# Kernel optimization log

Hardware: AMD Instinct MI355X
Metric: run time of the kernel (lower is better)

## Reference

```python
import jax, jax.numpy as jnp
import numpy as np

B, S, E, H = 4, 1024, 1024, 16
HD = E // H
TEMP = float(E) ** 0.5


def setup_inputs() -> dict:
    key = jax.random.key(0)
    ks = jax.random.split(key, 6)
    x = jax.random.normal(ks[0], (B, S, E), dtype=jnp.float32)
    mask = jax.random.randint(ks[1], (1, 1, S, S), 0, 2).astype(bool)
    prev = jax.random.normal(ks[2], (B, H, S, S), dtype=jnp.float32)
    qkv_w = jax.random.normal(ks[3], (3 * E, E), dtype=jnp.float32) * (1.0 / np.sqrt(E))
    qkv_b = jnp.zeros((3 * E,), dtype=jnp.float32)
    o_w = jax.random.normal(ks[4], (E, E), dtype=jnp.float32) * (1.0 / np.sqrt(E))
    o_b = jnp.zeros((E,), dtype=jnp.float32)
    return {"x": x, "mask": mask, "prev": prev, "qkv_w": qkv_w,
            "qkv_b": qkv_b, "o_w": o_w, "o_b": o_b}


def reference(x, mask, prev, qkv_w, qkv_b, o_w, o_b):
    b, s, _ = x.shape
    # qkv_proj: torch Linear -> x @ W^T + b, then per-head interleaved split
    qkv = x @ qkv_w.T + qkv_b                      # [B, S, 3E]
    qkv = qkv.reshape(b, s, H, 3 * HD).transpose(0, 2, 1, 3)  # [B, H, S, 3*HD]
    q, k, v = jnp.split(qkv, 3, axis=-1)           # each [B, H, S, HD]
    attn = jnp.einsum('bhqd,bhkd->bhqk', q, k) / TEMP + prev  # raw scores
    attn = jnp.where(mask, -jnp.inf, attn)         # masked_fill(mask, -inf)
    p = jax.nn.softmax(attn, axis=-1)              # dropout p=0 (eval)
    vals = jnp.einsum('bhqk,bhkd->bhqd', p, v)     # [B, H, S, HD]
    vals = vals.transpose(0, 2, 1, 3).reshape(b, s, E)
    return vals @ o_w.T + o_b
```

## Files before the change

kernel.cpp:

```cpp
#include <hip/hip_runtime.h>

typedef unsigned short u16;
typedef unsigned char  u8;
typedef unsigned long long u64;

using bf16x8 = __attribute__((ext_vector_type(8))) short;
using f32x4  = __attribute__((ext_vector_type(4))) float;

static __device__ __forceinline__ u16 f2bf(float f) {
  union { float f; unsigned u; } v; v.f = f;
  unsigned r = v.u + 0x7fffu + ((v.u >> 16) & 1u);
  return (u16)(r >> 16);
}

static __device__ __forceinline__ void gload_lds16(const void* g, void* l) {
  __builtin_amdgcn_global_load_lds((const __attribute__((address_space(1))) void*)g,
                                   (__attribute__((address_space(3))) void*)l, 16, 0, 0);
}

__global__ __launch_bounds__(256) void cvt_bf16_kernel(const float4* __restrict__ in,
                                                       ushort4* __restrict__ out, int n4) {
  int i = blockIdx.x * 256 + threadIdx.x;
  if (i >= n4) return;
  float4 v = in[i];
  ushort4 o;
  o.x = f2bf(v.x); o.y = f2bf(v.y); o.z = f2bf(v.z); o.w = f2bf(v.w);
  out[i] = o;
}

__global__ __launch_bounds__(256) void zero_out_kernel(float* __restrict__ out, int n) {
  int i = blockIdx.x * 256 + threadIdx.x;
  if (i < n) out[i] = 0.f;
}

__global__ void mask_detect_kernel(const u8* __restrict__ mask, int* __restrict__ flag) {
  __shared__ int nz;
  if (threadIdx.x == 0) nz = 0;
  __syncthreads();
  int cnt = 0;
  for (int i = threadIdx.x; i < 4096; i += 256)
    if ((i & 3) && mask[i]) cnt++;
  if (cnt) atomicAdd(&nz, cnt);
  __syncthreads();
  if (threadIdx.x == 0) *flag = (nz == 0) ? 1 : 0;
}

__global__ __launch_bounds__(256) void mask_pack_kernel(const void* __restrict__ mask,
                                                        u64* __restrict__ out,
                                                        const int* __restrict__ flag, int nwords) {
  int w = blockIdx.x * 4 + (threadIdx.x >> 6);
  int lane = threadIdx.x & 63;
  if (w >= nwords) return;
  int idx = w * 64 + lane;
  int m;
  if (*flag) m = ((const int*)mask)[idx] != 0;
  else       m = ((const u8*)mask)[idx] != 0;
  u64 bits = __ballot(m != 0);
  if (lane == 0) out[w] = bits;
}

template<bool OUT_BF16>
__global__ __launch_bounds__(256, 2)
void gemm_bt(const u16* __restrict__ A, const u16* __restrict__ Bm,
             const float* __restrict__ bias, void* __restrict__ Cout,
             int M, int N, int K) {
  constexpr int BK = 64;
  __shared__ u16 lA[128 * BK];
  __shared__ u16 lB[128 * BK];
  const int tid = threadIdx.x;
  const int wv = tid >> 6, lane = tid & 63;
  const int wr = (wv >> 1) * 64, wc = (wv & 1) * 64;
  const int bm = blockIdx.x * 128, bn = blockIdx.y * 128;
  const int frow = lane & 15, fk = (lane >> 4) * 8;
  const int srow = tid >> 3;
  const int scol = (tid & 7) * 8;
  const u16* ga = A + (size_t)(bm + srow) * K + scol;
  const u16* gb = Bm + (size_t)(bn + srow) * K + scol;
  u16* la = &lA[srow * BK + scol];
  u16* lb = &lB[srow * BK + scol];

  f32x4 acc[4][4] = {};

  for (int k0 = 0; k0 < K; k0 += BK) {
#pragma unroll
    for (int r = 0; r < 4; ++r) {
      gload_lds16(ga + (size_t)(r * 32) * K + k0, la + r * 32 * BK);
      gload_lds16(gb + (size_t)(r * 32) * K + k0, lb + r * 32 * BK);
    }
    __syncthreads();
#pragma unroll
    for (int kk = 0; kk < 2; ++kk) {
      bf16x8 af[4], bf[4];
#pragma unroll
      for (int m = 0; m < 4; ++m)
        af[m] = *(const bf16x8*)&lA[(wr + m * 16 + frow) * BK + kk * 32 + fk];
#pragma unroll
      for (int n = 0; n < 4; ++n)
        bf[n] = *(const bf16x8*)&lB[(wc + n * 16 + frow) * BK + kk * 32 + fk];
#pragma unroll
      for (int m = 0; m < 4; ++m)
#pragma unroll
        for (int n = 0; n < 4; ++n)
          acc[m][n] = __builtin_amdgcn_mfma_f32_16x16x32_bf16(af[m], bf[n], acc[m][n], 0, 0, 0);
    }
    __syncthreads();
  }
#pragma unroll
  for (int n = 0; n < 4; ++n) {
    const int col = bn + wc + n * 16 + frow;
    const float bv = bias[col];
#pragma unroll
    for (int m = 0; m < 4; ++m) {
      const int row0 = bm + wr + m * 16 + (lane >> 4) * 4;
#pragma unroll
      for (int r = 0; r < 4; ++r) {
        float v = acc[m][n][r] + bv;
        if constexpr (OUT_BF16)
          ((u16*)Cout)[(size_t)(row0 + r) * N + col] = f2bf(v);
        else
          ((float*)Cout)[(size_t)(row0 + r) * N + col] = v;
      }
    }
  }
}

__global__ __launch_bounds__(256, 4)
void attn_kernel(const u16* __restrict__ qkv,
                 const float* __restrict__ prev,
                 const u64* __restrict__ mbits,
                 u16* __restrict__ vals) {
  constexpr int S = 1024;
  __shared__ u16 lQ[64 * 64];
  __shared__ u16 lK[64 * 64];
  __shared__ u16 lVT[64 * 64];
  __shared__ u16 lP[4][16 * 72];
  const int tid = threadIdx.x, wv = tid >> 6, lane = tid & 63;
  const int bh = blockIdx.x >> 4;
  const int qt = blockIdx.x & 15;
  const int b = bh >> 4, h = bh & 15;
  const int frow = lane & 15, fkg = lane >> 4, fk = fkg * 8;
  const int srow = tid >> 3, scol8 = (tid & 7) * 8;
  const size_t rowQ0 = (size_t)(b * S + qt * 64);

  const int scol_sw = scol8 ^ ((srow & 7) << 3);
  const int c0 = fk ^ ((frow & 7) << 3);
  const int c1 = (fk + 32) ^ ((frow & 7) << 3);

  {
    const u16* g = qkv + (rowQ0 + srow) * 3072 + h * 192 + scol_sw;
    gload_lds16(g, &lQ[srow * 64 + scol8]);
    gload_lds16(g + (size_t)32 * 3072, &lQ[(srow + 32) * 64 + scol8]);
  }
  __syncthreads();
  bf16x8 qf0 = *(const bf16x8*)&lQ[(wv * 16 + frow) * 64 + c0];
  bf16x8 qf1 = *(const bf16x8*)&lQ[(wv * 16 + frow) * 64 + c1];

  float m_run[4], l_run[4];
  f32x4 acc_o[4] = {};
#pragma unroll
  for (int r = 0; r < 4; ++r) { m_run[r] = -3e38f; l_run[r] = 0.f; }

  const int qloc = wv * 16 + fkg * 4;
  const float* prow = prev + ((size_t)bh * S + qt * 64 + qloc) * S;
  const u64* mrow = mbits + (size_t)(qt * 64 + qloc) * (S / 64);

  const int vsw = (tid & 7) << 3;

  for (int kt = 0; kt < 16; ++kt) {
    __syncthreads();
    {
      const u16* g = qkv + (size_t)(b * S + kt * 64 + srow) * 3072 + h * 192 + 64 + scol_sw;
      gload_lds16(g, &lK[srow * 64 + scol8]);
      gload_lds16(g + (size_t)32 * 3072, &lK[(srow + 32) * 64 + scol8]);
    }
    const u16* gv = qkv + (size_t)(b * S + kt * 64 + srow) * 3072 + h * 192 + 128 + scol8;
    bf16x8 v0 = *(const bf16x8*)gv;
    bf16x8 v1 = *(const bf16x8*)(gv + (size_t)32 * 3072);
    {
      const int k0 = srow ^ vsw;
      const int k1 = (srow + 32) ^ vsw;
#pragma unroll
      for (int j = 0; j < 8; ++j) {
        lVT[(scol8 + j) * 64 + k0] = (u16)v0[j];
        lVT[(scol8 + j) * 64 + k1] = (u16)v1[j];
      }
    }
    __syncthreads();
    const float* pp = prow + kt * 64 + frow;
    float pvraw[4][4];
    u64 mw[4];
#pragma unroll
    for (int r = 0; r < 4; ++r) mw[r] = mrow[r * (S / 64) + kt];
#pragma unroll
    for (int n = 0; n < 4; ++n)
#pragma unroll
      for (int r = 0; r < 4; ++r)
        pvraw[n][r] = pp[(size_t)r * S + n * 16];
    f32x4 s[4];
#pragma unroll
    for (int n = 0; n < 4; ++n) {
      bf16x8 kf0 = *(const bf16x8*)&lK[(n * 16 + frow) * 64 + c0];
      bf16x8 kf1 = *(const bf16x8*)&lK[(n * 16 + frow) * 64 + c1];
      f32x4 z = {0.f, 0.f, 0.f, 0.f};
      z = __builtin_amdgcn_mfma_f32_16x16x32_bf16(qf0, kf0, z, 0, 0, 0);
      s[n] = __builtin_amdgcn_mfma_f32_16x16x32_bf16(qf1, kf1, z, 0, 0, 0);
    }
#pragma unroll
    for (int r = 0; r < 4; ++r) {
      const u64 t = mw[r] >> frow;
#pragma unroll
      for (int n = 0; n < 4; ++n) {
        float sc = s[n][r] * 0.03125f + pvraw[n][r];
        s[n][r] = ((t >> (n * 16)) & 1ull) ? -1e30f : sc;
      }
    }
    float tmax[4];
#pragma unroll
    for (int r = 0; r < 4; ++r) {
      float t = fmaxf(fmaxf(s[0][r], s[1][r]), fmaxf(s[2][r], s[3][r]));
      t = fmaxf(t, __shfl_xor(t, 1));
      t = fmaxf(t, __shfl_xor(t, 2));
      t = fmaxf(t, __shfl_xor(t, 4));
      t = fmaxf(t, __shfl_xor(t, 8));
      tmax[r] = t;
    }
    float psum[4];
#pragma unroll
    for (int r = 0; r < 4; ++r) {
      float mnew = fmaxf(m_run[r], tmax[r]);
      float sc = __expf(m_run[r] - mnew);
      m_run[r] = mnew;
      l_run[r] *= sc;
#pragma unroll
      for (int dn = 0; dn < 4; ++dn) acc_o[dn][r] *= sc;
      float ps = 0.f;
#pragma unroll
      for (int n = 0; n < 4; ++n) {
        float p = __expf(s[n][r] - mnew);
        s[n][r] = p;
        ps += p;
      }
      psum[r] = ps;
    }
#pragma unroll
    for (int r = 0; r < 4; ++r) {
      float t = psum[r];
      t += __shfl_xor(t, 1); t += __shfl_xor(t, 2);
      t += __shfl_xor(t, 4); t += __shfl_xor(t, 8);
      l_run[r] += t;
    }
    u16* pw = &lP[wv][0];
#pragma unroll
    for (int n = 0; n < 4; ++n)
#pragma unroll
      for (int r = 0; r < 4; ++r)
        pw[(fkg * 4 + r) * 72 + n * 16 + frow] = f2bf(s[n][r]);
    bf16x8 pf0 = *(const bf16x8*)&pw[frow * 72 + fk];
    bf16x8 pf1 = *(const bf16x8*)&pw[frow * 72 + 32 + fk];
#pragma unroll
    for (int dn = 0; dn < 4; ++dn) {
      const int d = dn * 16 + frow;
      const int sw = ((dn * 2 + (frow >> 3)) & 7) << 3;
      bf16x8 vt0 = *(const bf16x8*)&lVT[d * 64 + (fk ^ sw)];
      bf16x8 vt1 = *(const bf16x8*)&lVT[d * 64 + ((fk + 32) ^ sw)];
      acc_o[dn] = __builtin_amdgcn_mfma_f32_16x16x32_bf16(pf0, vt0, acc_o[dn], 0, 0, 0);
      acc_o[dn] = __builtin_amdgcn_mfma_f32_16x16x32_bf16(pf1, vt1, acc_o[dn], 0, 0, 0);
    }
  }
#pragma unroll
  for (int r = 0; r < 4; ++r) {
    float inv = 1.0f / l_run[r];
    size_t row = (rowQ0 + qloc + r) * 1024 + h * 64;
#pragma unroll
    for (int dn = 0; dn < 4; ++dn)
      vals[row + dn * 16 + frow] = f2bf(acc_o[dn][r] * inv);
  }
}

extern "C" void kernel_launch(void* const* d_in, const int* in_sizes, int n_in,
                              void* d_out, int out_size, void* d_ws, size_t ws_size,
                              hipStream_t stream) {
  const float* x     = (const float*)d_in[0];
  const void*  mask  = d_in[1];
  const float* prev  = (const float*)d_in[2];
  const float* qkv_w = (const float*)d_in[3];
  const float* qkv_b = (const float*)d_in[4];
  const float* o_w   = (const float*)d_in[5];
  const float* o_b   = (const float*)d_in[6];

  const size_t WS_NEEDED = 14680064 + 25165824;
  if (ws_size < WS_NEEDED) {
    zero_out_kernel<<<(out_size + 255) / 256, 256, 0, stream>>>((float*)d_out, out_size);
    return;
  }

  char* ws = (char*)d_ws;
  u16* x_bf  = (u16*)(ws);
  u16* vals  = (u16*)(ws);
  u16* qw_bf   = (u16*)(ws + 8388608);
  u16* ow_bf   = (u16*)(ws + 8388608);
  u64* mask_b  = (u64*)(ws + 10485760);
  int* mflag   = (int*)(ws + 11534336);
  u16* qkv_o = (u16*)(ws + 14680064);

  cvt_bf16_kernel<<<4096, 256, 0, stream>>>((const float4*)x, (ushort4*)x_bf, 1048576);
  cvt_bf16_kernel<<<3072, 256, 0, stream>>>((const float4*)qkv_w, (ushort4*)qw_bf, 786432);

  dim3 g1(32, 24);
  gemm_bt<true><<<g1, 256, 0, stream>>>(x_bf, qw_bf, qkv_b, qkv_o, 4096, 3072, 1024);

  cvt_bf16_kernel<<<1024, 256, 0, stream>>>((const float4*)o_w, (ushort4*)ow_bf, 262144);
  mask_detect_kernel<<<1, 256, 0, stream>>>((const u8*)mask, mflag);
  mask_pack_kernel<<<4096, 256, 0, stream>>>(mask, mask_b, mflag, 16384);

  attn_kernel<<<1024, 256, 0, stream>>>(qkv_o, prev, mask_b, vals);

  dim3 g2(32, 8);
  gemm_bt<false><<<g2, 256, 0, stream>>>(vals, ow_bf, o_b, d_out, 4096, 1024, 1024);
}
```

Before: 508.8 us.

## Stage prev scores through LDS with async loads and fuse mask detect into pack

The attention kernel now loads each 64x64 tile of the fp32 prev bias into shared memory with async global-to-LDS 16-byte loads using an XOR swizzle, instead of scattered per-lane scalar global loads. This should make the dominant prev read traffic coalesced and let it overlap with the K/V tile loads. It adds 16KB of LDS per block, so the occupancy hint drops from 4 to 3 blocks. The separate single-block mask-detect launch is folded into the mask pack kernel, which redoes format detection locally in each block. This removes one launch and a serial dependency, and the packed mask moves to its own workspace region.

Result: no change. 517.9 us (+1.8%).

```diff
diff --git a/kernel.cpp b/kernel.cpp
--- a/kernel.cpp
+++ b/kernel.cpp
@@ -33,30 +33,21 @@
   if (i < n) out[i] = 0.f;
 }
 
-__global__ void mask_detect_kernel(const u8* __restrict__ mask, int* __restrict__ flag) {
+__global__ __launch_bounds__(256) void mask_pack_kernel(const void* __restrict__ mask,
+                                                        u64* __restrict__ out) {
   __shared__ int nz;
-  if (threadIdx.x == 0) nz = 0;
+  const int tid = threadIdx.x, b = blockIdx.x;
+  if (tid == 0) nz = 0;
   __syncthreads();
-  int cnt = 0;
-  for (int i = threadIdx.x; i < 4096; i += 256)
-    if ((i & 3) && mask[i]) cnt++;
-  if (cnt) atomicAdd(&nz, cnt);
+  const int idx = b * 256 + tid;
+  const u8 byte = ((const u8*)mask)[idx];
+  if ((idx & 3) && byte) atomicAdd(&nz, 1);
   __syncthreads();
-  if (threadIdx.x == 0) *flag = (nz == 0) ? 1 : 0;
-}
-
-__global__ __launch_bounds__(256) void mask_pack_kernel(const void* __restrict__ mask,
-                                                        u64* __restrict__ out,
-                                                        const int* __restrict__ flag, int nwords) {
-  int w = blockIdx.x * 4 + (threadIdx.x >> 6);
-  int lane = threadIdx.x & 63;
-  if (w >= nwords) return;
-  int idx = w * 64 + lane;
   int m;
-  if (*flag) m = ((const int*)mask)[idx] != 0;
-  else       m = ((const u8*)mask)[idx] != 0;
-  u64 bits = __ballot(m != 0);
-  if (lane == 0) out[w] = bits;
+  if (nz == 0) m = ((const int*)mask)[idx] != 0;
+  else         m = byte != 0;
+  u64 bits = __ballot(m);
+  if ((tid & 63) == 0) out[b * 4 + (tid >> 6)] = bits;
 }
 
 template<bool OUT_BF16>
@@ -124,7 +115,7 @@
   }
 }
 
-__global__ __launch_bounds__(256, 4)
+__global__ __launch_bounds__(256, 3)
 void attn_kernel(const u16* __restrict__ qkv,
                  const float* __restrict__ prev,
                  const u64* __restrict__ mbits,
@@ -134,6 +125,7 @@
   __shared__ u16 lK[64 * 64];
   __shared__ u16 lVT[64 * 64];
   __shared__ u16 lP[4][16 * 72];
+  __shared__ float lPrev[64 * 64];
   const int tid = threadIdx.x, wv = tid >> 6, lane = tid & 63;
   const int bh = blockIdx.x >> 4;
   const int qt = blockIdx.x & 15;
@@ -161,21 +153,31 @@
   for (int r = 0; r < 4; ++r) { m_run[r] = -3e38f; l_run[r] = 0.f; }
 
   const int qloc = wv * 16 + fkg * 4;
-  const float* prow = prev + ((size_t)bh * S + qt * 64 + qloc) * S;
   const u64* mrow = mbits + (size_t)(qt * 64 + qloc) * (S / 64);
+
+  const float* prevt = prev + ((size_t)bh * S + qt * 64) * S;
+  const int prow_s = wv * 4 + (lane >> 4);
+  const int pcolg = ((lane & 15) * 4) ^ (wv << 4);
+  const int prd = fkg << 4;
 
   const int vsw = (tid & 7) << 3;
 
   for (int kt = 0; kt < 16; ++kt) {
     __syncthreads();
+    const u16* gv = qkv + (size_t)(b * S + kt * 64 + srow) * 3072 + h * 192 + 128 + scol8;
+    bf16x8 v0 = *(const bf16x8*)gv;
+    bf16x8 v1 = *(const bf16x8*)(gv + (size_t)32 * 3072);
     {
       const u16* g = qkv + (size_t)(b * S + kt * 64 + srow) * 3072 + h * 192 + 64 + scol_sw;
       gload_lds16(g, &lK[srow * 64 + scol8]);
       gload_lds16(g + (size_t)32 * 3072, &lK[(srow + 32) * 64 + scol8]);
     }
-    const u16* gv = qkv + (size_t)(b * S + kt * 64 + srow) * 3072 + h * 192 + 128 + scol8;
-    bf16x8 v0 = *(const bf16x8*)gv;
-    bf16x8 v1 = *(const bf16x8*)(gv + (size_t)32 * 3072);
+    {
+      const float* p0 = prevt + (size_t)kt * 64 + pcolg;
+#pragma unroll
+      for (int i = 0; i < 4; ++i)
+        gload_lds16(p0 + (size_t)(i * 16 + prow_s) * S, &lPrev[(i * 256 + tid) * 4]);
+    }
     {
       const int k0 = srow ^ vsw;
       const int k1 = (srow + 32) ^ vsw;
@@ -186,16 +188,9 @@
       }
     }
     __syncthreads();
-    const float* pp = prow + kt * 64 + frow;
-    float pvraw[4][4];
     u64 mw[4];
 #pragma unroll
     for (int r = 0; r < 4; ++r) mw[r] = mrow[r * (S / 64) + kt];
-#pragma unroll
-    for (int n = 0; n < 4; ++n)
-#pragma unroll
-      for (int r = 0; r < 4; ++r)
-        pvraw[n][r] = pp[(size_t)r * S + n * 16];
     f32x4 s[4];
 #pragma unroll
     for (int n = 0; n < 4; ++n) {
@@ -208,9 +203,11 @@
 #pragma unroll
     for (int r = 0; r < 4; ++r) {
       const u64 t = mw[r] >> frow;
+      const int prbase = (qloc + r) * 64;
 #pragma unroll
       for (int n = 0; n < 4; ++n) {
-        float sc = s[n][r] * 0.03125f + pvraw[n][r];
+        float pv = lPrev[prbase + ((n * 16 + frow) ^ prd)];
+        float sc = s[n][r] * 0.03125f + pv;
         s[n][r] = ((t >> (n * 16)) & 1ull) ? -1e30f : sc;
       }
     }
@@ -288,7 +285,7 @@
   const float* o_w   = (const float*)d_in[5];
   const float* o_b   = (const float*)d_in[6];
 
-  const size_t WS_NEEDED = 14680064 + 25165824;
+  const size_t WS_NEEDED = 41943040 + 131072;
   if (ws_size < WS_NEEDED) {
     zero_out_kernel<<<(out_size + 255) / 256, 256, 0, stream>>>((float*)d_out, out_size);
     return;
@@ -297,12 +294,12 @@
   char* ws = (char*)d_ws;
   u16* x_bf  = (u16*)(ws);
   u16* vals  = (u16*)(ws);
-  u16* qw_bf   = (u16*)(ws + 8388608);
-  u16* ow_bf   = (u16*)(ws + 8388608);
-  u64* mask_b  = (u64*)(ws + 10485760);
-  int* mflag   = (int*)(ws + 11534336);
+  u16* qw_bf = (u16*)(ws + 8388608);
+  u16* ow_bf = (u16*)(ws + 8388608);
   u16* qkv_o = (u16*)(ws + 14680064);
-
+  u64* mask_b = (u64*)(ws + 41943040);
+
+  mask_pack_kernel<<<4096, 256, 0, stream>>>(mask, mask_b);
   cvt_bf16_kernel<<<4096, 256, 0, stream>>>((const float4*)x, (ushort4*)x_bf, 1048576);
   cvt_bf16_kernel<<<3072, 256, 0, stream>>>((const float4*)qkv_w, (ushort4*)qw_bf, 786432);
 
@@ -310,8 +307,6 @@
   gemm_bt<true><<<g1, 256, 0, stream>>>(x_bf, qw_bf, qkv_b, qkv_o, 4096, 3072, 1024);
 
   cvt_bf16_kernel<<<1024, 256, 0, stream>>>((const float4*)o_w, (ushort4*)ow_bf, 262144);
-  mask_detect_kernel<<<1, 256, 0, stream>>>((const u8*)mask, mflag);
-  mask_pack_kernel<<<4096, 256, 0, stream>>>(mask, mask_b, mflag, 16384);
 
   attn_kernel<<<1024, 256, 0, stream>>>(qkv_o, prev, mask_b, vals);
 
```
